# Kernel optimization log

Measured on AMD Instinct MI355X. Metric: run time of the kernel, lower is better.

## Reference

```python
import jax, jax.numpy as jnp
import numpy as np

H = 128; W = 128; WH = 8; WW = 8; SH = 4; SW = 4
DIM = 512; HEADS = 16; HD = DIM // HEADS; HIDDEN = 2048
NH = H // WH; NW = W // WW; NWIN = NH * NW; WL = WH * WW
EPS = 1e-5
SCALE = HD ** -0.5


def _rel_pos_index():
    # Swin-style relative position index, static (WL, WL) int table
    coords = np.stack(np.meshgrid(np.arange(WH), np.arange(WW), indexing='ij')).reshape(2, -1)
    rel = (coords[:, :, None] - coords[:, None, :]).transpose(1, 2, 0)  # (WL, WL, 2)
    rel[:, :, 0] += WH - 1
    rel[:, :, 1] += WW - 1
    rel[:, :, 0] *= 2 * WW - 1
    return rel.sum(-1)  # (WL, WL), values in [0, (2WH-1)(2WW-1))


def _shift_attn_mask():
    # static shifted-window attention mask, (NWIN, WL, WL)
    m = np.zeros((H, W))
    cnt = 0
    for hs in (slice(0, -WH), slice(-WH, -SH), slice(-SH, None)):
        for ws in (slice(0, -WW), slice(-WW, -SW), slice(-SW, None)):
            m[hs, ws] = cnt
            cnt += 1
    mw = m.reshape(NH, WH, NW, WW).transpose(0, 2, 1, 3).reshape(NWIN, WL)
    am = mw[:, None, :] - mw[:, :, None]
    return np.where(am != 0, -100.0, 0.0).astype(np.float32)


_RPI = _rel_pos_index()
_MASK = _shift_attn_mask()


def _layernorm(x, w, b):
    mu = x.mean(-1, keepdims=True)
    var = ((x - mu) ** 2).mean(-1, keepdims=True)
    return (x - mu) / jnp.sqrt(var + EPS) * w + b


def _win_part(x):  # (H, W, D) -> (NWIN, WL, D)
    return x.reshape(NH, WH, NW, WW, DIM).transpose(0, 2, 1, 3, 4).reshape(NWIN, WL, DIM)


def _win_rev(w):  # (NWIN, WL, D) -> (H, W, D)
    return w.reshape(NH, NW, WH, WW, DIM).transpose(0, 2, 1, 3, 4).reshape(H, W, DIM)


def setup_inputs() -> dict:
    key = jax.random.key(0)
    ks = jax.random.split(key, 8)
    s = 0.02
    return {
        'x': jax.random.normal(ks[0], (H * W, DIM), dtype=jnp.float32),
        'ln1_w': jnp.ones((DIM,), jnp.float32),
        'ln1_b': jnp.zeros((DIM,), jnp.float32),
        'ln2_w': jnp.ones((DIM,), jnp.float32),
        'ln2_b': jnp.zeros((DIM,), jnp.float32),
        'qkv_w': jax.random.normal(ks[1], (3 * DIM, DIM), dtype=jnp.float32) * s,
        'qkv_b': jnp.zeros((3 * DIM,), jnp.float32),
        'proj_w': jax.random.normal(ks[2], (DIM, DIM), dtype=jnp.float32) * s,
        'proj_b': jnp.zeros((DIM,), jnp.float32),
        'rpb': jax.random.normal(ks[3], ((2 * WH - 1) * (2 * WW - 1), HEADS), dtype=jnp.float32) * s,
        'mlp_w1': jax.random.normal(ks[4], (HIDDEN, DIM), dtype=jnp.float32) * s,
        'mlp_b1': jnp.zeros((HIDDEN,), jnp.float32),
        'mlp_w2': jax.random.normal(ks[5], (DIM, HIDDEN), dtype=jnp.float32) * s,
        'mlp_b2': jnp.zeros((DIM,), jnp.float32),
    }


def reference(x, ln1_w, ln1_b, ln2_w, ln2_b, qkv_w, qkv_b, proj_w, proj_b, rpb,
              mlp_w1, mlp_b1, mlp_w2, mlp_b2):
    skip = x
    h = _layernorm(x, ln1_w, ln1_b).reshape(H, W, DIM)
    # cyclic shift + window partition
    h = jnp.roll(h, shift=(-SH, -SW), axis=(0, 1))
    xw = _win_part(h)  # (NWIN, WL, DIM)
    # windowed multi-head self-attention (equinox Linear: y = W @ x + b)
    qkv = jnp.einsum('nld,ed->nle', xw, qkv_w) + qkv_b
    q, k, v = [t.reshape(NWIN, WL, HEADS, HD).transpose(0, 2, 1, 3)
               for t in jnp.split(qkv, 3, axis=-1)]  # each (NWIN, HEADS, WL, HD)
    attn = jnp.einsum('nhqd,nhkd->nhqk', q * SCALE, k)
    bias = rpb[_RPI.reshape(-1)].reshape(WL, WL, HEADS).transpose(2, 0, 1)  # (HEADS, WL, WL)
    attn = attn + bias[None] + jnp.asarray(_MASK)[:, None]
    attn = jax.nn.softmax(attn, axis=-1)
    out = jnp.einsum('nhqk,nhkd->nhqd', attn, v).transpose(0, 2, 1, 3).reshape(NWIN, WL, DIM)
    out = jnp.einsum('nld,ed->nle', out, proj_w) + proj_b
    # window reverse + reverse cyclic shift
    h = jnp.roll(_win_rev(out), shift=(SH, SW), axis=(0, 1)).reshape(H * W, DIM)
    h = skip + h  # residual (drop_path is Identity at rate 0)
    # FFN branch (note: original code does x = x + drop_path(x), i.e. 2*mlp(norm2(.)))
    h = _layernorm(h, ln2_w, ln2_b)
    m = jax.nn.gelu(jnp.einsum('ld,ed->le', h, mlp_w1) + mlp_b1)
    m = jnp.einsum('le,de->ld', m, mlp_w2) + mlp_b2
    return m + m
```

## Files before the change

kernel.cpp:

```cpp
#include <hip/hip_runtime.h>
#include <hip/hip_bf16.h>
#include <stdint.h>

#define TOK   16384
#define DIMM  512
#define NHEAD 16
#define HDIM  32
#define HID   2048
#define NWIN  256
#define WLEN  64
#define EPSV  1e-5f
#define SCL   0.17677669529663687f

typedef __hip_bfloat16 bf16;
typedef __attribute__((ext_vector_type(8))) __bf16 bf16x8;
typedef __attribute__((ext_vector_type(4))) float f32x4;

__device__ __forceinline__ int remap_row(int r){
  int win = r >> 6, l = r & 63;
  int gh = ((win >> 4) << 3) + (l >> 3);
  int gw = ((win & 15) << 3) + (l & 7);
  int oh = (gh + 4) & 127, ow = (gw + 4) & 127;
  return (oh << 7) + ow;
}

__device__ __forceinline__ int region_of(int win, int l){
  int gh = ((win >> 4) << 3) + (l >> 3);
  int gw = ((win & 15) << 3) + (l & 7);
  int rh = (gh < 120) ? 0 : ((gh < 124) ? 1 : 2);
  int rw = (gw < 120) ? 0 : ((gw < 124) ? 1 : 2);
  return rh * 3 + rw;
}

__device__ __forceinline__ void gl_lds16(const bf16* g, bf16* l){
  __builtin_amdgcn_global_load_lds((const __attribute__((address_space(1))) void*)g,
                                   (__attribute__((address_space(3))) void*)l, 16, 0, 0);
}

__global__ __launch_bounds__(256) void convert_w(const float* __restrict__ a,
                                                 const float* __restrict__ b,
                                                 const float* __restrict__ c,
                                                 const float* __restrict__ d,
                                                 bf16* __restrict__ dst){
  int e = (blockIdx.x * 256 + threadIdx.x) * 4;
  float4 v;
  if (e < 786432)        v = *(const float4*)(a + e);
  else if (e < 1048576)  v = *(const float4*)(b + (e - 786432));
  else if (e < 2097152)  v = *(const float4*)(c + (e - 1048576));
  else                   v = *(const float4*)(d + (e - 2097152));
  union { bf16 h[4]; int2 q; } u;
  u.h[0] = __float2bfloat16(v.x); u.h[1] = __float2bfloat16(v.y);
  u.h[2] = __float2bfloat16(v.z); u.h[3] = __float2bfloat16(v.w);
  *(int2*)(dst + e) = u.q;
}

template<bool REMAP>
__global__ __launch_bounds__(256) void ln_kernel(const float* __restrict__ in,
    const float* __restrict__ w, const float* __restrict__ b, bf16* __restrict__ outp)
{
  const int wave = threadIdx.x >> 6, lane = threadIdx.x & 63;
  const int r = blockIdx.x * 4 + wave;
  const int src = REMAP ? remap_row(r) : r;
  const float4* row = (const float4*)(in + (size_t)src * DIMM);
  float4 v0 = row[lane*2], v1 = row[lane*2 + 1];
  float sm = v0.x+v0.y+v0.z+v0.w + v1.x+v1.y+v1.z+v1.w;
  float sq = v0.x*v0.x+v0.y*v0.y+v0.z*v0.z+v0.w*v0.w
           + v1.x*v1.x+v1.y*v1.y+v1.z*v1.z+v1.w*v1.w;
  #pragma unroll
  for (int off = 1; off < 64; off <<= 1){
    sm += __shfl_xor(sm, off);
    sq += __shfl_xor(sq, off);
  }
  const float mean = sm * (1.f/512.f);
  const float rstd = rsqrtf(sq*(1.f/512.f) - mean*mean + EPSV);
  const float4* wp = (const float4*)w; const float4* bp = (const float4*)b;
  float4 w0 = wp[lane*2], w1 = wp[lane*2+1], b0 = bp[lane*2], b1 = bp[lane*2+1];
  union { bf16 h[8]; int4 q; } u;
  u.h[0] = __float2bfloat16((v0.x-mean)*rstd*w0.x + b0.x);
  u.h[1] = __float2bfloat16((v0.y-mean)*rstd*w0.y + b0.y);
  u.h[2] = __float2bfloat16((v0.z-mean)*rstd*w0.z + b0.z);
  u.h[3] = __float2bfloat16((v0.w-mean)*rstd*w0.w + b0.w);
  u.h[4] = __float2bfloat16((v1.x-mean)*rstd*w1.x + b1.x);
  u.h[5] = __float2bfloat16((v1.y-mean)*rstd*w1.y + b1.y);
  u.h[6] = __float2bfloat16((v1.z-mean)*rstd*w1.z + b1.z);
  u.h[7] = __float2bfloat16((v1.w-mean)*rstd*w1.w + b1.w);
  *(int4*)(outp + (size_t)r*DIMM + lane*8) = u.q;
}

#define M_QKV  0
#define M_PROJ 1
#define M_MLP1 2
#define M_MLP2 3
#define M_PART 4

template<int MODE, int K>
__global__ __launch_bounds__(256) void gemm_bt(const bf16* __restrict__ A,
    const bf16* __restrict__ Wt, const float* __restrict__ bias,
    bf16* __restrict__ out_b, float* __restrict__ out_f, const float* __restrict__ skip)
{
  __shared__ bf16 lsA[2][128*32];
  __shared__ bf16 lsB[2][128*32];
  const int tid = threadIdx.x, wave = tid >> 6, lane = tid & 63;
  const int lrow = lane & 15, lgrp = lane >> 4;
  const int m0 = blockIdx.x * 128, n0 = blockIdx.y * 128;
  const int wr = (wave >> 1) * 64, wc = (wave & 1) * 64;

  f32x4 acc[4][4] = {};

  const bf16* Abase = A  + (size_t)m0 * K;
  const bf16* Bbase = Wt + (size_t)n0 * K;
  const int srow = tid >> 2;
  const int scol = (tid & 3) * 8;

  #define STAGE(kt, bf) { \
    gl_lds16(Abase + (size_t)(srow)      * K + (kt) + scol, lsA[bf] + wave*512); \
    gl_lds16(Abase + (size_t)(srow + 64) * K + (kt) + scol, lsA[bf] + 2048 + wave*512); \
    gl_lds16(Bbase + (size_t)(srow)      * K + (kt) + scol, lsB[bf] + wave*512); \
    gl_lds16(Bbase + (size_t)(srow + 64) * K + (kt) + scol, lsB[bf] + 2048 + wave*512); \
  }

  STAGE(0, 0);
  __syncthreads();
  int cur = 0;
  for (int kt = 0; kt < K; kt += 32){
    if (kt + 32 < K) STAGE(kt + 32, cur ^ 1);
    bf16x8 af[4], bfv[4];
    #pragma unroll
    for (int i = 0; i < 4; i++){
      af[i]  = *(const bf16x8*)(lsA[cur] + (wr + i*16 + lrow)*32 + lgrp*8);
      bfv[i] = *(const bf16x8*)(lsB[cur] + (wc + i*16 + lrow)*32 + lgrp*8);
    }
    #pragma unroll
    for (int i = 0; i < 4; i++)
      #pragma unroll
      for (int j = 0; j < 4; j++)
        acc[i][j] = __builtin_amdgcn_mfma_f32_16x16x32_bf16(af[i], bfv[j], acc[i][j], 0, 0, 0);
    __syncthreads();
    cur ^= 1;
  }
  #undef STAGE

  #pragma unroll
  for (int i = 0; i < 4; i++){
    #pragma unroll
    for (int j = 0; j < 4; j++){
      const int col   = n0 + wc + j*16 + lrow;
      const int row_b = m0 + wr + i*16 + lgrp*4;
      const float bv = bias[col];
      #pragma unroll
      for (int rr = 0; rr < 4; rr++){
        const int row = row_b + rr;
        float v = acc[i][j][rr] + bv;
        if constexpr (MODE == M_PROJ){
          const int o = remap_row(row);
          out_f[(size_t)o*DIMM + col] = v + skip[(size_t)o*DIMM + col];
        } else {
          out_f[(size_t)row*DIMM + col] = v;
        }
      }
    }
  }
}

template<int KSTR>
__device__ __forceinline__ void stage_ht(const bf16* __restrict__ P,
                                         int grow0, bf16* lbase, int tid, int kt){
  const int r = tid >> 3;
  const int c = ((tid & 7) ^ (r & 7)) * 8;
  const bf16* g = P + (size_t)(grow0 + r) * KSTR + kt * 64 + c;
  bf16* l = lbase + r * 64 + (tid & 7) * 8;
  gl_lds16(g, l);
  gl_lds16(g + (size_t)64 * KSTR, l + 4096);
}

template<int MODE, int KEXT, int KSTR = KEXT>
__global__ __launch_bounds__(512, 1) void gemm8_bt(const bf16* __restrict__ A,
    const bf16* __restrict__ Wt, const float* __restrict__ bias,
    bf16* __restrict__ out_b, float* __restrict__ out_f, float* __restrict__ out_f2)
{
  constexpr int NT = KEXT / 64;
  extern __shared__ bf16 lds[];
  bf16* As = lds;
  bf16* Bs = lds + 32768;
  const int tid = threadIdx.x;
  const int ln = tid & 63, wv = tid >> 6;
  const int lrow = ln & 15, lgrp = ln >> 4;
  const int swz = lrow & 7;
  const int wm = wv >> 2, wn = wv & 3;
  const int m0 = blockIdx.x * 256, n0 = blockIdx.y * 256;

  if constexpr (MODE == M_PART){
    A  += blockIdx.z * 1024;
    Wt += blockIdx.z * 1024;
  }

  f32x4 acc[8][4] = {};
  bf16x8 aA0[4][2], aA1[4][2], bB0[2][2], bB1[2][2];

  #define LDA(DST, MH) { _Pragma("unroll") for (int mf = 0; mf < 4; mf++) \
    _Pragma("unroll") for (int ks = 0; ks < 2; ks++) \
      DST[mf][ks] = *(const bf16x8*)(As + s*16384 + (wm*128 + (MH)*64 + mf*16 + lrow)*64 + ((ks*4 + lgrp) ^ swz)*8); }
  #define LDB(DST, NH) { _Pragma("unroll") for (int nf = 0; nf < 2; nf++) \
    _Pragma("unroll") for (int ks = 0; ks < 2; ks++) \
      DST[nf][ks] = *(const bf16x8*)(Bs + s*16384 + (wn*64 + (NH)*32 + nf*16 + lrow)*64 + ((ks*4 + lgrp) ^ swz)*8); }
  #define QUAD(AR, BR, IM0, JN0) { _Pragma("unroll") for (int ks = 0; ks < 2; ks++) \
    _Pragma("unroll") for (int mf = 0; mf < 4; mf++) \
      _Pragma("unroll") for (int nf = 0; nf < 2; nf++) \
        acc[(IM0)+mf][(JN0)+nf] = __builtin_amdgcn_mfma_f32_16x16x32_bf16(AR[mf][ks], BR[nf][ks], acc[(IM0)+mf][(JN0)+nf], 0, 0, 0); }
  #define SBAR() { __builtin_amdgcn_sched_barrier(0); __builtin_amdgcn_s_barrier(); __builtin_amdgcn_sched_barrier(0); }

  stage_ht<KSTR>(A,  m0,       As,        tid, 0);
  stage_ht<KSTR>(Wt, n0,       Bs,        tid, 0);
  stage_ht<KSTR>(Wt, n0 + 128, Bs + 8192, tid, 0);
  stage_ht<KSTR>(A,  m0 + 128, As + 8192, tid, 0);
  asm volatile("s_waitcnt vmcnt(0)" ::: "memory");
  SBAR();
  stage_ht<KSTR>(A, m0,       As + 16384,        tid, 1);
  stage_ht<KSTR>(A, m0 + 128, As + 16384 + 8192, tid, 1);

  for (int t = 0; t < NT; ++t){
    const int s = t & 1;
    const int sx = s ^ 1;
    LDA(aA0, 0); LDB(bB0, 0); LDA(aA1, 1);
    if (t + 1 < NT){
      stage_ht<KSTR>(Wt, n0,       Bs + sx*16384,        tid, t + 1);
      stage_ht<KSTR>(Wt, n0 + 128, Bs + sx*16384 + 8192, tid, t + 1);
    }
    __builtin_amdgcn_s_setprio(1);
    QUAD(aA0, bB0, 0, 0);
    QUAD(aA1, bB0, 4, 0);
    __builtin_amdgcn_s_setprio(0);
    SBAR();
    LDB(bB1, 1);
    if (t + 2 < NT){
      stage_ht<KSTR>(A, m0,       As + s*16384,        tid, t + 2);
      stage_ht<KSTR>(A, m0 + 128, As + s*16384 + 8192, tid, t + 2);
    }
    __builtin_amdgcn_s_setprio(1);
    QUAD(aA0, bB1, 0, 2);
    QUAD(aA1, bB1, 4, 2);
    __builtin_amdgcn_s_setprio(0);
    if (t == NT - 2)      { asm volatile("s_waitcnt vmcnt(0)" ::: "memory"); }
    else if (t < NT - 2)  { asm volatile("s_waitcnt vmcnt(4)" ::: "memory"); }
    SBAR();
  }
  #undef LDA
  #undef LDB
  #undef QUAD
  #undef SBAR

  bf16* pdstb = nullptr;
  if constexpr (MODE == M_PART)
    pdstb = blockIdx.z ? (bf16*)out_f2 : (bf16*)out_f;
  #pragma unroll
  for (int im = 0; im < 8; im++){
    #pragma unroll
    for (int jn = 0; jn < 4; jn++){
      const int col = n0 + wn*64 + (jn >> 1)*32 + (jn & 1)*16 + lrow;
      const int row_b = m0 + wm*128 + (im >> 2)*64 + (im & 3)*16 + lgrp*4;
      const float bv = (MODE == M_PART) ? 0.f : bias[col];
      #pragma unroll
      for (int rr = 0; rr < 4; rr++){
        const int row = row_b + rr;
        float v = acc[im][jn][rr] + bv;
        if constexpr (MODE == M_QKV){
          const int t = col >> 9, rem = col & 511;
          const int head = rem >> 5, hd = rem & 31;
          const int win = row >> 6, l = row & 63;
          out_b[(size_t)t * (TOK*DIMM) + ((size_t)(win*NHEAD + head)*WLEN + l)*HDIM + hd]
              = __float2bfloat16(v);
        } else if constexpr (MODE == M_MLP1){
          const float u = 1.5957691216057308f * (v + 0.044715f*v*v*v);
          const float g = v * (1.0f / (1.0f + __expf(-u)));
          out_b[(size_t)row*HID + col] = __float2bfloat16(g);
        } else if constexpr (MODE == M_PART){
          pdstb[(size_t)row*DIMM + col] = __float2bfloat16(v);
        } else {
          out_f[(size_t)row*DIMM + col] = 2.f * v;
        }
      }
    }
  }
}

__global__ __launch_bounds__(256) void mlp2_reduce(const bf16* __restrict__ p0,
    const bf16* __restrict__ p1, float* __restrict__ dout, const float* __restrict__ bias){
  const size_t i = (size_t)(blockIdx.x * 256 + threadIdx.x) * 8;
  int4 a = *(const int4*)(p0 + i);
  int4 b = *(const int4*)(p1 + i);
  const int cb = (int)(i & 511);
  const float4 bv0 = *(const float4*)(bias + cb);
  const float4 bv1 = *(const float4*)(bias + cb + 4);
  const bf16* ah = (const bf16*)&a;
  const bf16* bh = (const bf16*)&b;
  float4 r0, r1;
  r0.x = 2.f*(__bfloat162float(ah[0]) + __bfloat162float(bh[0]) + bv0.x);
  r0.y = 2.f*(__bfloat162float(ah[1]) + __bfloat162float(bh[1]) + bv0.y);
  r0.z = 2.f*(__bfloat162float(ah[2]) + __bfloat162float(bh[2]) + bv0.z);
  r0.w = 2.f*(__bfloat162float(ah[3]) + __bfloat162float(bh[3]) + bv0.w);
  r1.x = 2.f*(__bfloat162float(ah[4]) + __bfloat162float(bh[4]) + bv1.x);
  r1.y = 2.f*(__bfloat162float(ah[5]) + __bfloat162float(bh[5]) + bv1.y);
  r1.z = 2.f*(__bfloat162float(ah[6]) + __bfloat162float(bh[6]) + bv1.z);
  r1.w = 2.f*(__bfloat162float(ah[7]) + __bfloat162float(bh[7]) + bv1.w);
  *(float4*)(dout + i)     = r0;
  *(float4*)(dout + i + 4) = r1;
}

__global__ __launch_bounds__(256) void attn_kernel(const bf16* __restrict__ qkv,
    const float* __restrict__ rpb, bf16* __restrict__ outp)
{
  __shared__ bf16 Pl[4][64][72];
  const int wave = threadIdx.x >> 6, lane = threadIdx.x & 63;
  const int lrow = lane & 15, lgrp = lane >> 4;
  const int wh = blockIdx.x * 4 + wave;
  const int win = wh >> 4, head = wh & 15;
  const bf16* qb = qkv + (size_t)wh * (WLEN*HDIM);
  const bf16* kb = qb + (size_t)TOK * DIMM;
  const bf16* vb = kb + (size_t)TOK * DIMM;

  bf16x8 aq[4], ak[4];
  #pragma unroll
  for (int i = 0; i < 4; i++){
    aq[i] = *(const bf16x8*)(qb + (i*16 + lrow)*HDIM + lgrp*8);
    ak[i] = *(const bf16x8*)(kb + (i*16 + lrow)*HDIM + lgrp*8);
  }
  f32x4 s[4][4] = {};
  #pragma unroll
  for (int i = 0; i < 4; i++)
    #pragma unroll
    for (int j = 0; j < 4; j++)
      s[i][j] = __builtin_amdgcn_mfma_f32_16x16x32_bf16(aq[i], ak[j], s[i][j], 0, 0, 0);

  #pragma unroll
  for (int i = 0; i < 4; i++){
    #pragma unroll
    for (int rr = 0; rr < 4; rr++){
      const int srow = i*16 + lgrp*4 + rr;
      const int rq = region_of(win, srow);
      float vals[4]; float mx = -1e30f;
      #pragma unroll
      for (int j = 0; j < 4; j++){
        const int scol = j*16 + lrow;
        const int idx = ((srow>>3) - (scol>>3) + 7)*15 + ((srow&7) - (scol&7) + 7);
        float v = s[i][j][rr]*SCL + rpb[idx*NHEAD + head];
        if (region_of(win, scol) != rq) v -= 100.f;
        vals[j] = v; mx = fmaxf(mx, v);
      }
      mx = fmaxf(mx, __shfl_xor(mx, 1));
      mx = fmaxf(mx, __shfl_xor(mx, 2));
      mx = fmaxf(mx, __shfl_xor(mx, 4));
      mx = fmaxf(mx, __shfl_xor(mx, 8));
      float sum = 0.f;
      #pragma unroll
      for (int j = 0; j < 4; j++){ vals[j] = __expf(vals[j] - mx); sum += vals[j]; }
      sum += __shfl_xor(sum, 1); sum += __shfl_xor(sum, 2);
      sum += __shfl_xor(sum, 4); sum += __shfl_xor(sum, 8);
      const float rs = 1.f / sum;
      #pragma unroll
      for (int j = 0; j < 4; j++)
        Pl[wave][srow][j*16 + lrow] = __float2bfloat16(vals[j] * rs);
    }
  }

  f32x4 o[4][2] = {};
  const __bf16* vraw = (const __bf16*)vb;
  #pragma unroll
  for (int st = 0; st < 2; st++){
    bf16x8 pa[4];
    #pragma unroll
    for (int i = 0; i < 4; i++)
      pa[i] = *(const bf16x8*)(&Pl[wave][i*16 + lrow][st*32 + lgrp*8]);
    bf16x8 bv[2];
    #pragma unroll
    for (int j = 0; j < 2; j++){
      #pragma unroll
      for (int jj = 0; jj < 8; jj++)
        bv[j][jj] = vraw[(size_t)(st*32 + lgrp*8 + jj)*HDIM + j*16 + lrow];
    }
    #pragma unroll
    for (int i = 0; i < 4; i++)
      #pragma unroll
      for (int j = 0; j < 2; j++)
        o[i][j] = __builtin_amdgcn_mfma_f32_16x16x32_bf16(pa[i], bv[j], o[i][j], 0, 0, 0);
  }
  bf16* orow = outp + (size_t)win * WLEN * DIMM + head * HDIM;
  #pragma unroll
  for (int i = 0; i < 4; i++)
    #pragma unroll
    for (int j = 0; j < 2; j++)
      #pragma unroll
      for (int rr = 0; rr < 4; rr++){
        const int l = i*16 + lgrp*4 + rr;
        orow[(size_t)l * DIMM + j*16 + lrow] = __float2bfloat16(o[i][j][rr]);
      }
}

extern "C" void kernel_launch(void* const* d_in, const int* in_sizes, int n_in,
                              void* d_out, int out_size, void* d_ws, size_t ws_size,
                              hipStream_t stream) {
  const float* x     = (const float*)d_in[0];
  const float* ln1w  = (const float*)d_in[1];
  const float* ln1b  = (const float*)d_in[2];
  const float* ln2w  = (const float*)d_in[3];
  const float* ln2b  = (const float*)d_in[4];
  const float* qkvw  = (const float*)d_in[5];
  const float* qkvbi = (const float*)d_in[6];
  const float* projw = (const float*)d_in[7];
  const float* projb = (const float*)d_in[8];
  const float* rpb   = (const float*)d_in[9];
  const float* m1w   = (const float*)d_in[10];
  const float* m1b   = (const float*)d_in[11];
  const float* m2w   = (const float*)d_in[12];
  const float* m2b   = (const float*)d_in[13];

  bf16* wqkv  = (bf16*)d_ws;
  bf16* wproj = wqkv + 786432;
  bf16* wm1   = wproj + 262144;
  bf16* wm2   = wm1 + 1048576;
  bf16* xw    = wm2 + 1048576;
  float* hbuf = (float*)(xw + 8388608);
  bf16* qkvb  = (bf16*)(hbuf + 8388608);
  bf16* attno = qkvb + 3*(size_t)8388608;
  bf16* m1buf = qkvb;
  bf16* h2    = xw;

  hipFuncSetAttribute((const void*)&gemm8_bt<M_QKV, 512>,
                      hipFuncAttributeMaxDynamicSharedMemorySize, 131072);
  hipFuncSetAttribute((const void*)&gemm8_bt<M_MLP1, 512>,
                      hipFuncAttributeMaxDynamicSharedMemorySize, 131072);
  hipFuncSetAttribute((const void*)&gemm8_bt<M_PART, 1024, 2048>,
                      hipFuncAttributeMaxDynamicSharedMemorySize, 131072);

  convert_w<<<3072, 256, 0, stream>>>(qkvw, projw, m1w, m2w, wqkv);
  ln_kernel<true><<<4096, 256, 0, stream>>>(x, ln1w, ln1b, xw);
  { dim3 g(TOK/256, 1536/256);
    gemm8_bt<M_QKV, 512><<<g, 512, 131072, stream>>>(xw, wqkv, qkvbi, qkvb, nullptr, nullptr); }
  attn_kernel<<<1024, 256, 0, stream>>>(qkvb, rpb, attno);
  { dim3 g(TOK/128, 512/128);
    gemm_bt<M_PROJ, 512><<<g, 256, 0, stream>>>(attno, wproj, projb, nullptr, hbuf, x); }
  ln_kernel<false><<<4096, 256, 0, stream>>>(hbuf, ln2w, ln2b, h2);
  { dim3 g(TOK/256, 2048/256);
    gemm8_bt<M_MLP1, 512><<<g, 512, 131072, stream>>>(h2, wm1, m1b, m1buf, nullptr, nullptr); }
  { dim3 g(TOK/256, 512/256, 2);
    gemm8_bt<M_PART, 1024, 2048><<<g, 512, 131072, stream>>>(m1buf, wm2, m2b, nullptr,
                                                             (float*)hbuf, (float*)xw); }
  mlp2_reduce<<<8388608/8/256, 256, 0, stream>>>((const bf16*)hbuf, (const bf16*)xw,
                                                 (float*)d_out, m2b);
}
```

Measured before the change: 223.1 us.

## Reschedule GEMM main loop into four-quadrant pipeline and remap workgroup order

Restructures the GEMM K-loop so each iteration runs four MFMA quadrants separated by barriers, with explicit lgkmcnt waits and the global-to-LDS staging of A and B halves spread across the phases instead of two bulk stages. It also remaps the block index so consecutive workgroups are spread across groups of eight, which changes which tiles run together and so which A/B tiles are shared in cache. The aim is finer overlap of LDS reads, global loads and matrix math. The extra barriers per iteration and the hardcoded 64-tile M decomposition in the remap add risk, and the remap assumes a grid of 64 blocks along M.

Measured after the change: 228.8 us. +2.5%, slower.

```diff
diff --git a/kernel.cpp b/kernel.cpp
--- a/kernel.cpp
+++ b/kernel.cpp
@@ -187,7 +187,11 @@
   const int lrow = ln & 15, lgrp = ln >> 4;
   const int swz = lrow & 7;
   const int wm = wv >> 2, wn = wv & 3;
-  const int m0 = blockIdx.x * 256, n0 = blockIdx.y * 256;
+
+  const int nwg  = gridDim.x * gridDim.y;
+  const int orig = blockIdx.y * gridDim.x + blockIdx.x;
+  const int wgid = (orig & 7) * (nwg >> 3) + (orig >> 3);
+  const int m0 = (wgid & 63) * 256, n0 = (wgid >> 6) * 256;
 
   if constexpr (MODE == M_PART){
     A  += blockIdx.z * 1024;
@@ -208,6 +212,7 @@
       _Pragma("unroll") for (int nf = 0; nf < 2; nf++) \
         acc[(IM0)+mf][(JN0)+nf] = __builtin_amdgcn_mfma_f32_16x16x32_bf16(AR[mf][ks], BR[nf][ks], acc[(IM0)+mf][(JN0)+nf], 0, 0, 0); }
   #define SBAR() { __builtin_amdgcn_sched_barrier(0); __builtin_amdgcn_s_barrier(); __builtin_amdgcn_sched_barrier(0); }
+  #define LGKM(N) { asm volatile("s_waitcnt lgkmcnt(" #N ")" ::: "memory"); __builtin_amdgcn_sched_barrier(0); }
 
   stage_ht<KSTR>(A,  m0,       As,        tid, 0);
   stage_ht<KSTR>(Wt, n0,       Bs,        tid, 0);
@@ -215,39 +220,42 @@
   stage_ht<KSTR>(A,  m0 + 128, As + 8192, tid, 0);
   asm volatile("s_waitcnt vmcnt(0)" ::: "memory");
   SBAR();
-  stage_ht<KSTR>(A, m0,       As + 16384,        tid, 1);
-  stage_ht<KSTR>(A, m0 + 128, As + 16384 + 8192, tid, 1);
+  stage_ht<KSTR>(Wt, n0,       Bs + 16384,        tid, 1);
+  stage_ht<KSTR>(A,  m0,       As + 16384,        tid, 1);
+  stage_ht<KSTR>(Wt, n0 + 128, Bs + 16384 + 8192, tid, 1);
 
   for (int t = 0; t < NT; ++t){
     const int s = t & 1;
     const int sx = s ^ 1;
-    LDA(aA0, 0); LDB(bB0, 0); LDA(aA1, 1);
-    if (t + 1 < NT){
-      stage_ht<KSTR>(Wt, n0,       Bs + sx*16384,        tid, t + 1);
-      stage_ht<KSTR>(Wt, n0 + 128, Bs + sx*16384 + 8192, tid, t + 1);
-    }
-    __builtin_amdgcn_s_setprio(1);
-    QUAD(aA0, bB0, 0, 0);
-    QUAD(aA1, bB0, 4, 0);
-    __builtin_amdgcn_s_setprio(0);
+    LDA(aA0, 0); LDB(bB0, 0);
+    __builtin_amdgcn_sched_barrier(0);
+    LDB(bB1, 1);
+    if (t + 1 < NT) stage_ht<KSTR>(A, m0 + 128, As + sx*16384 + 8192, tid, t + 1);
+    LGKM(4);
+    __builtin_amdgcn_s_setprio(1); QUAD(aA0, bB0, 0, 0); __builtin_amdgcn_s_setprio(0);
     SBAR();
-    LDB(bB1, 1);
+    LDA(aA1, 1);
+    LGKM(8);
+    __builtin_amdgcn_s_setprio(1); QUAD(aA0, bB1, 0, 2); __builtin_amdgcn_s_setprio(0);
+    SBAR();
+    if (t + 2 < NT) stage_ht<KSTR>(Wt, n0, Bs + s*16384, tid, t + 2);
+    LGKM(0);
+    __builtin_amdgcn_s_setprio(1); QUAD(aA1, bB1, 4, 2); __builtin_amdgcn_s_setprio(0);
+    SBAR();
     if (t + 2 < NT){
-      stage_ht<KSTR>(A, m0,       As + s*16384,        tid, t + 2);
-      stage_ht<KSTR>(A, m0 + 128, As + s*16384 + 8192, tid, t + 2);
-    }
-    __builtin_amdgcn_s_setprio(1);
-    QUAD(aA0, bB1, 0, 2);
-    QUAD(aA1, bB1, 4, 2);
-    __builtin_amdgcn_s_setprio(0);
+      stage_ht<KSTR>(A,  m0,       As + s*16384,        tid, t + 2);
+      stage_ht<KSTR>(Wt, n0 + 128, Bs + s*16384 + 8192, tid, t + 2);
+    }
+    __builtin_amdgcn_s_setprio(1); QUAD(aA1, bB0, 4, 0); __builtin_amdgcn_s_setprio(0);
     if (t == NT - 2)      { asm volatile("s_waitcnt vmcnt(0)" ::: "memory"); }
-    else if (t < NT - 2)  { asm volatile("s_waitcnt vmcnt(4)" ::: "memory"); }
+    else if (t < NT - 2)  { asm volatile("s_waitcnt vmcnt(6)" ::: "memory"); }
     SBAR();
   }
   #undef LDA
   #undef LDB
   #undef QUAD
   #undef SBAR
+  #undef LGKM
 
   bf16* pdstb = nullptr;
   if constexpr (MODE == M_PART)
```
